# Optimization experiments

Measured on AMD Instinct MI355X. Metric: run time of the kernel, lower is better.

Reference implementation:

```python
import jax, jax.numpy as jnp
import numpy as np

B, Q, K, DQ, DK, H, DV = 4, 1024, 1024, 256, 256, 64, 256

def setup_inputs() -> dict:
    key = jax.random.key(0)
    k1, k2, k3, k4, k5, k6 = jax.random.split(key, 6)
    queries = jax.random.normal(k1, (B, Q, DQ), dtype=jnp.float32)
    keys = jax.random.normal(k2, (B, K, DK), dtype=jnp.float32)
    values = jax.random.normal(k3, (B, K, DV), dtype=jnp.float32)
    # learned params (stored as (in, out) so x @ W matches nn.Linear)
    W_q = jax.random.normal(k4, (DQ, H), dtype=jnp.float32) / np.sqrt(DQ)
    W_k = jax.random.normal(k5, (DK, H), dtype=jnp.float32) / np.sqrt(DK)
    w_v = jax.random.normal(k6, (H,), dtype=jnp.float32) / np.sqrt(H)
    return {"queries": queries, "keys": keys, "values": values,
            "W_q": W_q, "W_k": W_k, "w_v": w_v}

def reference(queries, keys, values, W_q, W_k, w_v):
    # projections: [B,Q,H], [B,K,H]
    q = jnp.einsum('bqd,dh->bqh', queries, W_q)
    k = jnp.einsum('bkd,dh->bkh', keys, W_k)
    # broadcast add -> tanh -> reduce with w_v: scores [B,Q,K]
    features = jnp.tanh(q[:, :, None, :] + k[:, None, :, :])  # [B,Q,K,H]
    scores = jnp.einsum('bqkh,h->bqk', features, w_v)
    attn = jax.nn.softmax(scores, axis=-1)  # dropout is identity in eval
    return jnp.einsum('bqk,bkv->bqv', attn, values)
```

## Files before the change

### kernel.cpp

```cpp
#include <hip/hip_runtime.h>

#define Bn 4
#define Qn 1024
#define Kn 1024
#define Dd 256
#define Hh 64
#define Dv 256
#define TQ 8

typedef __attribute__((ext_vector_type(8))) short short8;
typedef __attribute__((ext_vector_type(8))) _Float16 half8;
typedef __attribute__((ext_vector_type(4))) float floatx4;
typedef __attribute__((ext_vector_type(2))) float floatx2;

__device__ __forceinline__ floatx2 fma2(floatx2 a, floatx2 b, floatx2 c) {
    return __builtin_elementwise_fma(a, b, c);
}
__device__ __forceinline__ floatx2 mk2(float x, float y) {
    floatx2 r; r.x = x; r.y = y; return r;
}

__device__ __forceinline__ short f32_to_bf16(float x) {
    unsigned u = __float_as_uint(x);
    unsigned r = u + 0x7fffu + ((u >> 16) & 1u);
    return (short)(r >> 16);
}
__device__ __forceinline__ float bf16_to_f32(short h) {
    return __uint_as_float(((unsigned)(unsigned short)h) << 16);
}

__global__ __launch_bounds__(256) void prep_kernel(const float* __restrict__ Xq,
                                                   const float* __restrict__ Wq,
                                                   const float* __restrict__ Xk,
                                                   const float* __restrict__ Wk,
                                                   const float* __restrict__ V,
                                                   float* __restrict__ Eq,
                                                   float* __restrict__ Ekt,
                                                   _Float16* __restrict__ Vh) {
    __shared__ __align__(16) char smem[65536];
    int t = threadIdx.x;
    if (blockIdx.x < 128) {
        short* wh_lds = (short*)smem;
        short* wl_lds = (short*)(smem + 32768);
        int side = blockIdx.x >> 6;
        const float* X = side ? Xk : Xq;
        const float* W = side ? Wk : Wq;
        int wave = t >> 6, l = t & 63;
        int r0 = ((blockIdx.x & 63) * 4 + wave) * 16;
        const float* xrow = X + (size_t)(r0 + (l & 15)) * Dd + (l >> 4) * 8;
        floatx4 xa[8], xb[8];
        #pragma unroll
        for (int kt = 0; kt < 8; ++kt) {
            xa[kt] = *(const floatx4*)(xrow + kt * 32);
            xb[kt] = *(const floatx4*)(xrow + kt * 32 + 4);
        }
        #pragma unroll
        for (int si = 0; si < 8; ++si) {
            int s = si * 256 + t;
            int col = wave * 16 + (l & 15);
            int kb = si * 32 + (l >> 4) * 8;
            short8 hi, lo;
            #pragma unroll
            for (int j = 0; j < 8; ++j) {
                float x = W[(kb + j) * Hh + col];
                short hs = f32_to_bf16(x);
                hi[j] = hs;
                lo[j] = f32_to_bf16(x - bf16_to_f32(hs));
            }
            *(short8*)(wh_lds + s * 8) = hi;
            *(short8*)(wl_lds + s * 8) = lo;
        }
        __syncthreads();
        short8 ah[8], al[8];
        #pragma unroll
        for (int kt = 0; kt < 8; ++kt) {
            #pragma unroll
            for (int j = 0; j < 4; ++j) {
                short hs = f32_to_bf16(xa[kt][j]);
                ah[kt][j] = hs;
                al[kt][j] = f32_to_bf16(xa[kt][j] - bf16_to_f32(hs));
                short hs2 = f32_to_bf16(xb[kt][j]);
                ah[kt][j + 4] = hs2;
                al[kt][j + 4] = f32_to_bf16(xb[kt][j] - bf16_to_f32(hs2));
            }
        }
        floatx4 acc[4];
        #pragma unroll
        for (int ct = 0; ct < 4; ++ct) acc[ct] = (floatx4){0.f, 0.f, 0.f, 0.f};
        #pragma unroll
        for (int kt = 0; kt < 8; ++kt) {
            #pragma unroll
            for (int ct = 0; ct < 4; ++ct) {
                short8 wh = *(const short8*)(wh_lds + ((kt * 4 + ct) * 64 + l) * 8);
                short8 wl = *(const short8*)(wl_lds + ((kt * 4 + ct) * 64 + l) * 8);
                acc[ct] = __builtin_amdgcn_mfma_f32_16x16x32_bf16(ah[kt], wh, acc[ct], 0, 0, 0);
                acc[ct] = __builtin_amdgcn_mfma_f32_16x16x32_bf16(al[kt], wh, acc[ct], 0, 0, 0);
                acc[ct] = __builtin_amdgcn_mfma_f32_16x16x32_bf16(ah[kt], wl, acc[ct], 0, 0, 0);
            }
        }
        #pragma unroll
        for (int ct = 0; ct < 4; ++ct) {
            int h = ct * 16 + (l & 15);
            float e0 = __expf(2.f * acc[ct][0]);
            float e1 = __expf(2.f * acc[ct][1]);
            float e2 = __expf(2.f * acc[ct][2]);
            float e3 = __expf(2.f * acc[ct][3]);
            int row0g = r0 + (l >> 4) * 4;
            if (!side) {
                Eq[(size_t)(row0g + 0) * Hh + h] = e0;
                Eq[(size_t)(row0g + 1) * Hh + h] = e1;
                Eq[(size_t)(row0g + 2) * Hh + h] = e2;
                Eq[(size_t)(row0g + 3) * Hh + h] = e3;
            } else {
                int b = row0g >> 10, k0 = row0g & 1023;
                float4 o = { e0, e1, e2, e3 };
                *(float4*)(Ekt + ((size_t)(b * Hh + h)) * Kn + k0) = o;
            }
        }
    } else {
        float* tile = (float*)smem;
        int blk = blockIdx.x - 128;
        int b = blk >> 5;
        int kt = blk & 31;
        const float* Vg = V + (b * Kn + kt * 32) * Dv;
        for (int i = 0; i < 8; ++i) {
            int k = i * 4 + (t >> 6);
            int n4 = (t & 63) * 4;
            float4 v = *(const float4*)(Vg + k * Dv + n4);
            tile[k * 261 + n4 + 0] = v.x;
            tile[k * 261 + n4 + 1] = v.y;
            tile[k * 261 + n4 + 2] = v.z;
            tile[k * 261 + n4 + 3] = v.w;
        }
        __syncthreads();
        int wave = t >> 6, l = t & 63;
        int n_in = l & 15, kc = l >> 4;
        for (int p = 0; p < 4; ++p) {
            int nt = wave * 4 + p;
            int n = nt * 16 + n_in;
            half8 hi;
            #pragma unroll
            for (int j = 0; j < 8; ++j) {
                hi[j] = (_Float16)tile[(kc * 8 + j) * 261 + n];
            }
            size_t base = (((size_t)(b * 32 + kt) * 16 + nt) * 512) + (size_t)l * 8;
            *(half8*)(Vh + base) = hi;
        }
    }
}

__global__ __launch_bounds__(1024, 8) void attn_kernel(const float* __restrict__ Eq,
                                                       const float* __restrict__ Ekt,
                                                       const _Float16* __restrict__ Vh,
                                                       const float* __restrict__ wv,
                                                       float* __restrict__ out) {
    __shared__ __align__(16) unsigned sc[TQ * 1028];
    __shared__ float wsum[16 * TQ];
    __shared__ float rinv_s[TQ];

    int tid = threadIdx.x;
    int blk = blockIdx.x;
    int b = (blk & 7) >> 1;
    int tile = (blk >> 3) * 2 + (blk & 1);
    int qbase = tile * TQ;

    const float* kb = Ekt + (size_t)b * Hh * Kn;
    const float* qp = Eq + (size_t)(b * Qn + qbase) * Hh;
    const float4* wv4 = (const float4*)wv;
    floatx2 s2[TQ / 2];
    #pragma unroll
    for (int i = 0; i < TQ / 2; ++i) { s2[i].x = 0.f; s2[i].y = 0.f; }

    float e0 = kb[0 * Kn + tid];
    float e1 = kb[1 * Kn + tid];
    float e2 = kb[2 * Kn + tid];
    float e3 = kb[3 * Kn + tid];
    floatx2 one2 = mk2(1.f, 1.f);
    for (int h4 = 0; h4 < Hh / 4; ++h4) {
        float n0, n1, n2, n3;
        if (h4 < Hh / 4 - 1) {
            const float* kn = kb + (h4 + 1) * 4 * Kn;
            n0 = kn[0 * Kn + tid];
            n1 = kn[1 * Kn + tid];
            n2 = kn[2 * Kn + tid];
            n3 = kn[3 * Kn + tid];
        }
        float4 w4 = wv4[h4];
        floatx2 e0s = mk2(e0, e0), e1s = mk2(e1, e1);
        floatx2 e2s = mk2(e2, e2), e3s = mk2(e3, e3);
        floatx2 wx = mk2(w4.x, w4.x), wy = mk2(w4.y, w4.y);
        floatx2 wz = mk2(w4.z, w4.z), ww = mk2(w4.w, w4.w);
        #pragma unroll
        for (int qq = 0; qq < TQ; qq += 2) {
            float4 qva = *(const float4*)(qp + qq * Hh + h4 * 4);
            float4 qvb = *(const float4*)(qp + (qq + 1) * Hh + h4 * 4);
            floatx2 A = fma2(mk2(qva.x, qvb.x), e0s, one2);
            floatx2 B = fma2(mk2(qva.y, qvb.y), e1s, one2);
            floatx2 C = fma2(mk2(qva.z, qvb.z), e2s, one2);
            floatx2 D = fma2(mk2(qva.w, qvb.w), e3s, one2);
            floatx2 AB = A * B;
            floatx2 CD = C * D;
            floatx2 ABCD = AB * CD;
            floatx2 NAB = fma2(wx, B, wy * A);
            floatx2 NCD = fma2(wz, D, ww * C);
            floatx2 NUM = fma2(NCD, AB, NAB * CD);
            floatx2 R = mk2(__builtin_amdgcn_rcpf(ABCD.x),
                            __builtin_amdgcn_rcpf(ABCD.y));
            s2[qq >> 1] = fma2(NUM, R, s2[qq >> 1]);
        }
        e0 = n0; e1 = n1; e2 = n2; e3 = n3;
    }

    _Float16* sp = (_Float16*)sc;
    float part[TQ];
    #pragma unroll
    for (int q = 0; q < TQ; ++q) {
        float sq = (q & 1) ? s2[q >> 1].y : s2[q >> 1].x;
        float p = __expf(-2.f * sq);
        part[q] = p;
        _Float16 hs = (_Float16)p;
        sp[q * 2056 + tid] = hs;
        sp[q * 2056 + 1024 + tid] = (_Float16)(p - (float)hs);
    }

    int wave = tid >> 6, lane = tid & 63;
    #pragma unroll
    for (int q = 0; q < TQ; ++q) {
        #pragma unroll
        for (int off = 32; off >= 1; off >>= 1)
            part[q] += __shfl_xor(part[q], off, 64);
    }
    if (lane == 0) {
        #pragma unroll
        for (int q = 0; q < TQ; ++q) wsum[wave * TQ + q] = part[q];
    }
    __syncthreads();

    if (wave < TQ) {
        float v = (lane < 16) ? wsum[lane * TQ + wave] : 0.f;
        v += __shfl_xor(v, 8, 64);
        v += __shfl_xor(v, 4, 64);
        v += __shfl_xor(v, 2, 64);
        v += __shfl_xor(v, 1, 64);
        if (lane == 0) rinv_s[wave] = 1.f / v;
    }
    __syncthreads();

    int qf = lane & 15, kc = lane >> 4;
    int qd = qf & (TQ - 1);
    floatx4 acc = {0.f, 0.f, 0.f, 0.f};
    const char* scb = (const char*)sc;
    for (int kt = 0; kt < 32; ++kt) {
        half8 bhi = *(const half8*)(scb + qd * 4112 + kt * 64 + kc * 16);
        half8 blo = *(const half8*)(scb + qd * 4112 + 2048 + kt * 64 + kc * 16);
        size_t base = (((size_t)(b * 32 + kt) * 16 + wave) * 512) + (size_t)lane * 8;
        half8 ah = *(const half8*)(Vh + base);
        acc = __builtin_amdgcn_mfma_f32_16x16x32_f16(ah, bhi, acc, 0, 0, 0);
        acc = __builtin_amdgcn_mfma_f32_16x16x32_f16(ah, blo, acc, 0, 0, 0);
    }
    if (qf < TQ) {
        float r = rinv_s[qd];
        float* ob = out + ((size_t)(b * Qn + qbase + qf)) * Dv + wave * 16 + kc * 4;
        float4 o = { acc[0] * r, acc[1] * r, acc[2] * r, acc[3] * r };
        *(float4*)ob = o;
    }
}

extern "C" void kernel_launch(void* const* d_in, const int* in_sizes, int n_in,
                              void* d_out, int out_size, void* d_ws, size_t ws_size,
                              hipStream_t stream) {
    const float* queries = (const float*)d_in[0];
    const float* keys    = (const float*)d_in[1];
    const float* values  = (const float*)d_in[2];
    const float* W_q     = (const float*)d_in[3];
    const float* W_k     = (const float*)d_in[4];
    const float* w_v     = (const float*)d_in[5];
    float* out = (float*)d_out;

    float* Eq  = (float*)d_ws;
    float* Ekt = Eq + Bn * Qn * Hh;
    _Float16* Vh = (_Float16*)(Ekt + Bn * Kn * Hh);

    prep_kernel<<<256, 256, 0, stream>>>(queries, W_q, keys, W_k, values,
                                         Eq, Ekt, Vh);
    attn_kernel<<<Bn * (Qn / TQ), 1024, 0, stream>>>(Eq, Ekt, Vh, w_v, out);
}
```

Baseline: 110.8 us.

## Drop LDS staging in prep, prefetch V in attention, remove sync

The projection part of prep_kernel now gives each wave its own 16-column tile of the weight, loaded and split into bf16 hi/lo in registers with no LDS. The grid grows from 256 to 640 blocks. The V conversion reads global memory directly instead of transposing through LDS. In attn_kernel the V fragment for the next k-tile is software-prefetched, and the softmax-denominator reduction is done per thread from wsum, which removes one __syncthreads. The trade-off is redundant weight loads and conversions per block, plus uncoalesced strided V reads.

```diff
diff --git a/kernel.cpp b/kernel.cpp
--- a/kernel.cpp
+++ b/kernel.cpp
@@ -37,16 +37,14 @@
                                                    float* __restrict__ Eq,
                                                    float* __restrict__ Ekt,
                                                    _Float16* __restrict__ Vh) {
-    __shared__ __align__(16) char smem[65536];
     int t = threadIdx.x;
-    if (blockIdx.x < 128) {
-        short* wh_lds = (short*)smem;
-        short* wl_lds = (short*)(smem + 32768);
-        int side = blockIdx.x >> 6;
+    int wave = t >> 6, l = t & 63;
+    if (blockIdx.x < 512) {
+        int side = blockIdx.x >> 8;
+        int r0 = (blockIdx.x & 255) * 16;
+        int ct = wave;
         const float* X = side ? Xk : Xq;
         const float* W = side ? Wk : Wq;
-        int wave = t >> 6, l = t & 63;
-        int r0 = ((blockIdx.x & 63) * 4 + wave) * 16;
         const float* xrow = X + (size_t)(r0 + (l & 15)) * Dd + (l >> 4) * 8;
         floatx4 xa[8], xb[8];
         #pragma unroll
@@ -54,24 +52,14 @@
             xa[kt] = *(const floatx4*)(xrow + kt * 32);
             xb[kt] = *(const floatx4*)(xrow + kt * 32 + 4);
         }
-        #pragma unroll
-        for (int si = 0; si < 8; ++si) {
-            int s = si * 256 + t;
-            int col = wave * 16 + (l & 15);
-            int kb = si * 32 + (l >> 4) * 8;
-            short8 hi, lo;
-            #pragma unroll
-            for (int j = 0; j < 8; ++j) {
-                float x = W[(kb + j) * Hh + col];
-                short hs = f32_to_bf16(x);
-                hi[j] = hs;
-                lo[j] = f32_to_bf16(x - bf16_to_f32(hs));
-            }
-            *(short8*)(wh_lds + s * 8) = hi;
-            *(short8*)(wl_lds + s * 8) = lo;
-        }
-        __syncthreads();
-        short8 ah[8], al[8];
+        float wraw[8][8];
+        #pragma unroll
+        for (int kt = 0; kt < 8; ++kt) {
+            const float* wp = W + (size_t)(kt * 32 + (l >> 4) * 8) * Hh + ct * 16 + (l & 15);
+            #pragma unroll
+            for (int j = 0; j < 8; ++j) wraw[kt][j] = wp[j * Hh];
+        }
+        short8 ah[8], al[8], wh[8], wl[8];
         #pragma unroll
         for (int kt = 0; kt < 8; ++kt) {
             #pragma unroll
@@ -83,68 +71,51 @@
                 ah[kt][j + 4] = hs2;
                 al[kt][j + 4] = f32_to_bf16(xb[kt][j] - bf16_to_f32(hs2));
             }
-        }
-        floatx4 acc[4];
-        #pragma unroll
-        for (int ct = 0; ct < 4; ++ct) acc[ct] = (floatx4){0.f, 0.f, 0.f, 0.f};
-        #pragma unroll
-        for (int kt = 0; kt < 8; ++kt) {
-            #pragma unroll
-            for (int ct = 0; ct < 4; ++ct) {
-                short8 wh = *(const short8*)(wh_lds + ((kt * 4 + ct) * 64 + l) * 8);
-                short8 wl = *(const short8*)(wl_lds + ((kt * 4 + ct) * 64 + l) * 8);
-                acc[ct] = __builtin_amdgcn_mfma_f32_16x16x32_bf16(ah[kt], wh, acc[ct], 0, 0, 0);
-                acc[ct] = __builtin_amdgcn_mfma_f32_16x16x32_bf16(al[kt], wh, acc[ct], 0, 0, 0);
-                acc[ct] = __builtin_amdgcn_mfma_f32_16x16x32_bf16(ah[kt], wl, acc[ct], 0, 0, 0);
+            #pragma unroll
+            for (int j = 0; j < 8; ++j) {
+                short hs = f32_to_bf16(wraw[kt][j]);
+                wh[kt][j] = hs;
+                wl[kt][j] = f32_to_bf16(wraw[kt][j] - bf16_to_f32(hs));
             }
         }
-        #pragma unroll
-        for (int ct = 0; ct < 4; ++ct) {
-            int h = ct * 16 + (l & 15);
-            float e0 = __expf(2.f * acc[ct][0]);
-            float e1 = __expf(2.f * acc[ct][1]);
-            float e2 = __expf(2.f * acc[ct][2]);
-            float e3 = __expf(2.f * acc[ct][3]);
-            int row0g = r0 + (l >> 4) * 4;
-            if (!side) {
-                Eq[(size_t)(row0g + 0) * Hh + h] = e0;
-                Eq[(size_t)(row0g + 1) * Hh + h] = e1;
-                Eq[(size_t)(row0g + 2) * Hh + h] = e2;
-                Eq[(size_t)(row0g + 3) * Hh + h] = e3;
-            } else {
-                int b = row0g >> 10, k0 = row0g & 1023;
-                float4 o = { e0, e1, e2, e3 };
-                *(float4*)(Ekt + ((size_t)(b * Hh + h)) * Kn + k0) = o;
-            }
+        floatx4 acc = {0.f, 0.f, 0.f, 0.f};
+        #pragma unroll
+        for (int kt = 0; kt < 8; ++kt) {
+            acc = __builtin_amdgcn_mfma_f32_16x16x32_bf16(ah[kt], wh[kt], acc, 0, 0, 0);
+            acc = __builtin_amdgcn_mfma_f32_16x16x32_bf16(al[kt], wh[kt], acc, 0, 0, 0);
+            acc = __builtin_amdgcn_mfma_f32_16x16x32_bf16(ah[kt], wl[kt], acc, 0, 0, 0);
+        }
+        int h = ct * 16 + (l & 15);
+        float e0 = __expf(2.f * acc[0]);
+        float e1 = __expf(2.f * acc[1]);
+        float e2 = __expf(2.f * acc[2]);
+        float e3 = __expf(2.f * acc[3]);
+        int row0g = r0 + (l >> 4) * 4;
+        if (!side) {
+            Eq[(size_t)(row0g + 0) * Hh + h] = e0;
+            Eq[(size_t)(row0g + 1) * Hh + h] = e1;
+            Eq[(size_t)(row0g + 2) * Hh + h] = e2;
+            Eq[(size_t)(row0g + 3) * Hh + h] = e3;
+        } else {
+            int b = row0g >> 10, k0 = row0g & 1023;
+            float4 o = { e0, e1, e2, e3 };
+            *(float4*)(Ekt + ((size_t)(b * Hh + h)) * Kn + k0) = o;
         }
     } else {
-        float* tile = (float*)smem;
-        int blk = blockIdx.x - 128;
-        int b = blk >> 5;
-        int kt = blk & 31;
-        const float* Vg = V + (b * Kn + kt * 32) * Dv;
-        for (int i = 0; i < 8; ++i) {
-            int k = i * 4 + (t >> 6);
-            int n4 = (t & 63) * 4;
-            float4 v = *(const float4*)(Vg + k * Dv + n4);
-            tile[k * 261 + n4 + 0] = v.x;
-            tile[k * 261 + n4 + 1] = v.y;
-            tile[k * 261 + n4 + 2] = v.z;
-            tile[k * 261 + n4 + 3] = v.w;
-        }
-        __syncthreads();
-        int wave = t >> 6, l = t & 63;
-        int n_in = l & 15, kc = l >> 4;
+        int vblk = blockIdx.x - 512;
+        int b = vblk >> 5;
+        int kt = vblk & 31;
+        const float* Vg = V + ((size_t)(b * Kn + kt * 32 + (l >> 4) * 8)) * Dv + (l & 15);
+        #pragma unroll
         for (int p = 0; p < 4; ++p) {
             int nt = wave * 4 + p;
-            int n = nt * 16 + n_in;
-            half8 hi;
-            #pragma unroll
-            for (int j = 0; j < 8; ++j) {
-                hi[j] = (_Float16)tile[(kc * 8 + j) * 261 + n];
-            }
+            const float* vp = Vg + nt * 16;
+            half8 hv;
+            #pragma unroll
+            for (int j = 0; j < 8; ++j)
+                hv[j] = (_Float16)vp[(size_t)j * Dv];
             size_t base = (((size_t)(b * 32 + kt) * 16 + nt) * 512) + (size_t)l * 8;
-            *(half8*)(Vh + base) = hi;
+            *(half8*)(Vh + base) = hv;
         }
     }
 }
@@ -156,7 +127,6 @@
                                                        float* __restrict__ out) {
     __shared__ __align__(16) unsigned sc[TQ * 1028];
     __shared__ float wsum[16 * TQ];
-    __shared__ float rinv_s[TQ];
 
     int tid = threadIdx.x;
     int blk = blockIdx.x;
@@ -211,6 +181,10 @@
         e0 = n0; e1 = n1; e2 = n2; e3 = n3;
     }
 
+    int wave = tid >> 6, lane = tid & 63;
+    size_t vb0 = (((size_t)(b * 32) * 16 + wave) * 512) + (size_t)lane * 8;
+    half8 vcur = *(const half8*)(Vh + vb0);
+
     _Float16* sp = (_Float16*)sc;
     float part[TQ];
     #pragma unroll
@@ -223,7 +197,6 @@
         sp[q * 2056 + 1024 + tid] = (_Float16)(p - (float)hs);
     }
 
-    int wave = tid >> 6, lane = tid & 63;
     #pragma unroll
     for (int q = 0; q < TQ; ++q) {
         #pragma unroll
@@ -233,33 +206,33 @@
     if (lane == 0) {
         #pragma unroll
         for (int q = 0; q < TQ; ++q) wsum[wave * TQ + q] = part[q];
-    }
-    __syncthreads();
-
-    if (wave < TQ) {
-        float v = (lane < 16) ? wsum[lane * TQ + wave] : 0.f;
-        v += __shfl_xor(v, 8, 64);
-        v += __shfl_xor(v, 4, 64);
-        v += __shfl_xor(v, 2, 64);
-        v += __shfl_xor(v, 1, 64);
-        if (lane == 0) rinv_s[wave] = 1.f / v;
     }
     __syncthreads();
 
     int qf = lane & 15, kc = lane >> 4;
     int qd = qf & (TQ - 1);
     floatx4 acc = {0.f, 0.f, 0.f, 0.f};
-    const char* scb = (const char*)sc;
-    for (int kt = 0; kt < 32; ++kt) {
-        half8 bhi = *(const half8*)(scb + qd * 4112 + kt * 64 + kc * 16);
-        half8 blo = *(const half8*)(scb + qd * 4112 + 2048 + kt * 64 + kc * 16);
-        size_t base = (((size_t)(b * 32 + kt) * 16 + wave) * 512) + (size_t)lane * 8;
-        half8 ah = *(const half8*)(Vh + base);
-        acc = __builtin_amdgcn_mfma_f32_16x16x32_f16(ah, bhi, acc, 0, 0, 0);
-        acc = __builtin_amdgcn_mfma_f32_16x16x32_f16(ah, blo, acc, 0, 0, 0);
+    const char* scb = (const char*)sc + qd * 4112 + kc * 16;
+    #pragma unroll 2
+    for (int kt = 0; kt < 31; ++kt) {
+        half8 vnext = *(const half8*)(Vh + vb0 + (size_t)(kt + 1) * 8192);
+        half8 bhi = *(const half8*)(scb + kt * 64);
+        half8 blo = *(const half8*)(scb + 2048 + kt * 64);
+        acc = __builtin_amdgcn_mfma_f32_16x16x32_f16(vcur, bhi, acc, 0, 0, 0);
+        acc = __builtin_amdgcn_mfma_f32_16x16x32_f16(vcur, blo, acc, 0, 0, 0);
+        vcur = vnext;
+    }
+    {
+        half8 bhi = *(const half8*)(scb + 31 * 64);
+        half8 blo = *(const half8*)(scb + 2048 + 31 * 64);
+        acc = __builtin_amdgcn_mfma_f32_16x16x32_f16(vcur, bhi, acc, 0, 0, 0);
+        acc = __builtin_amdgcn_mfma_f32_16x16x32_f16(vcur, blo, acc, 0, 0, 0);
     }
     if (qf < TQ) {
-        float r = rinv_s[qd];
+        float vsum = 0.f;
+        #pragma unroll
+        for (int w = 0; w < 16; ++w) vsum += wsum[w * TQ + qd];
+        float r = 1.f / vsum;
         float* ob = out + ((size_t)(b * Qn + qbase + qf)) * Dv + wave * 16 + kc * 4;
         float4 o = { acc[0] * r, acc[1] * r, acc[2] * r, acc[3] * r };
         *(float4*)ob = o;
@@ -281,7 +254,7 @@
     float* Ekt = Eq + Bn * Qn * Hh;
     _Float16* Vh = (_Float16*)(Ekt + Bn * Kn * Hh);
 
-    prep_kernel<<<256, 256, 0, stream>>>(queries, W_q, keys, W_k, values,
+    prep_kernel<<<640, 256, 0, stream>>>(queries, W_q, keys, W_k, values,
                                          Eq, Ekt, Vh);
     attn_kernel<<<Bn * (Qn / TQ), 1024, 0, stream>>>(Eq, Ekt, Vh, w_v, out);
 }
```

Result: no change. 110.2 us (-0.6%).
